# Kernel optimization log

Hardware: AMD Instinct MI355X
Metric: run time of the kernel (lower is better)

## Reference

```python
import jax, jax.numpy as jnp
import numpy as np

K, d = 8, 8
D = K * d          # 64
B, T, N = 8, 12, 325


def _xavier(key, shape):
    fan_out, fan_in = shape
    lim = (6.0 / (fan_in + fan_out)) ** 0.5
    return jax.random.uniform(key, shape, jnp.float32, -lim, lim)


def setup_inputs() -> dict:
    key = jax.random.key(0)
    ks = jax.random.split(key, 8)
    return {
        "X": jax.random.normal(ks[0], (B, T, N, D), jnp.float32),
        "STE": jax.random.normal(ks[1], (B, T, N, D), jnp.float32),
        "adj": jax.random.randint(ks[2], (N, N), 0, 2, jnp.int32),
        "W7": _xavier(ks[3], (D, 2 * D)), "b7": jnp.zeros((D,), jnp.float32),
        "W8": _xavier(ks[4], (D, 2 * D)), "b8": jnp.zeros((D,), jnp.float32),
        "W9": _xavier(ks[5], (D, 2 * D)), "b9": jnp.zeros((D,), jnp.float32),
        "W10": _xavier(ks[6], (D, D)), "b10": jnp.zeros((D,), jnp.float32),
        "W11": _xavier(ks[7], (D, D)), "b11": jnp.zeros((D,), jnp.float32),
    }


def reference(X, STE, adj, W7, b7, W8, b8, W9, b9, W10, b10, W11, b11):
    # X, STE: [B, T, N, D]
    x = jnp.concatenate([X, STE], axis=-1)  # [B,T,N,2D]
    gelu = lambda t: jax.nn.gelu(t, approximate=False)  # torch F.gelu default = exact erf
    q = gelu(x @ W7.T + b7)  # [B,T,N,D]
    k = gelu(x @ W8.T + b8)
    v = gelu(x @ W9.T + b9)
    # split D into K heads of size d (equivalent to torch split(dim=-1)+cat(dim=0))
    heads = lambda t: t.reshape(B, T, N, K, d)
    q, k, v = heads(q), heads(k), heads(v)
    # scores: [K,B,T,N,N] == torch's [K*B,T,N,N]
    attn = jnp.einsum('btnkd,btmkd->kbtnm', q, k) / (d ** 0.5)
    attn = jnp.where(adj > 0, attn, jnp.float32(-9e15))
    attn = jax.nn.softmax(attn, axis=-1)
    out = jnp.einsum('kbtnm,btmkd->btnkd', attn, v).reshape(B, T, N, D)
    out = gelu(out @ W10.T + b10) @ W11.T + b11
    return out
```

## Files before the change

kernel.cpp:

```cpp
#include <hip/hip_runtime.h>
#include <math.h>

#define NN 325
#define BT 96
#define NROWS (BT * NN)
#define SCL (0.35355339059327373f * 1.4426950408889634f)
#define QKV_BLKS ((NROWS + 63) / 64)
#define PREP_ITEMS (11 * NN + 8192)
#define PREP_BLKS ((PREP_ITEMS + 511) / 512)
#define TOT_BLKS (QKV_BLKS + PREP_BLKS)

typedef _Float16 half_t;
typedef half_t half8_t __attribute__((ext_vector_type(8)));
typedef half_t half4_t __attribute__((ext_vector_type(4)));
typedef half_t half2_t __attribute__((ext_vector_type(2)));
typedef float float4_t __attribute__((ext_vector_type(4)));

__device__ __forceinline__ float gelu_f(float x) {
    return 0.5f * x * (1.0f + erff(x * 0.70710678118654752f));
}

#define XS 136
#define PS 72

__device__ __forceinline__ void qkv_stage_wf(const float* __restrict__ src,
                                             half_t* dst, int tid)
{
    #pragma unroll
    for (int idx = tid; idx < 1024; idx += 512) {
        int c = idx >> 4, g = idx & 15;
        const float4* s4 = (const float4*)&src[c * 128 + g * 8];
        float4 a = s4[0], b = s4[1];
        half8_t h;
        h[0] = (half_t)a.x; h[1] = (half_t)a.y;
        h[2] = (half_t)a.z; h[3] = (half_t)a.w;
        h[4] = (half_t)b.x; h[5] = (half_t)b.y;
        h[6] = (half_t)b.z; h[7] = (half_t)b.w;
        *(half8_t*)&dst[c * XS + g * 8] = h;
    }
}

__device__ __forceinline__ void qkv_compute(
    const half_t* x16, const half_t* wb, const float* __restrict__ b,
    half_t* __restrict__ outp, float oscale,
    int row0, int rbase, int ch, int l15, int quad)
{
    float4_t acc[2];
    #pragma unroll
    for (int cc = 0; cc < 2; ++cc) {
        float bias = b[(ch * 2 + cc) * 16 + l15];
        acc[cc] = (float4_t){bias, bias, bias, bias};
    }
    #pragma unroll
    for (int kk = 0; kk < 8; ++kk) {
        half4_t a = *(const half4_t*)&x16[(rbase + l15) * XS + kk * 16 + quad * 4];
        #pragma unroll
        for (int cc = 0; cc < 2; ++cc) {
            half4_t bf = *(const half4_t*)
                &wb[((ch * 2 + cc) * 16 + l15) * XS + kk * 16 + quad * 4];
            acc[cc] = __builtin_amdgcn_mfma_f32_16x16x16f16(a, bf, acc[cc], 0, 0, 0);
        }
    }
    #pragma unroll
    for (int cc = 0; cc < 2; ++cc) {
        #pragma unroll
        for (int rr = 0; rr < 4; ++rr) {
            int R = row0 + rbase + quad * 4 + rr;
            if (R < NROWS)
                outp[R * 64 + (ch * 2 + cc) * 16 + l15] =
                    (half_t)(gelu_f(acc[cc][rr]) * oscale);
        }
    }
}

__global__ __launch_bounds__(512) void qkv_kernel(
    const float* __restrict__ X, const float* __restrict__ STE,
    const int* __restrict__ adj,
    const float* __restrict__ W7, const float* __restrict__ b7,
    const float* __restrict__ W8, const float* __restrict__ b8,
    const float* __restrict__ W9, const float* __restrict__ b9,
    const float* __restrict__ W10, const float* __restrict__ W11,
    half_t* __restrict__ q, half_t* __restrict__ k, half_t* __restrict__ v,
    unsigned int* __restrict__ packedT, half_t* __restrict__ wab)
{
    const int tid = threadIdx.x;
    const int bx  = blockIdx.x;

    if (bx >= QKV_BLKS) {
        int idx = (bx - QKV_BLKS) * 512 + tid;
        if (idx < 11 * NN) {
            int w = idx / NN, n = idx - w * NN;
            unsigned int bits = 0u;
            #pragma unroll 8
            for (int j = 0; j < 32; ++j) {
                int m = w * 32 + j;
                if (m < NN && adj[n * NN + m] > 0) bits |= (1u << j);
            }
            packedT[w * NN + n] = bits;
        } else if (idx < PREP_ITEMS) {
            int i = idx - 11 * NN;
            int p = i >> 12, r = i & 4095;
            wab[i] = (half_t)(p ? W11[r] : W10[r]);
        }
        return;
    }

    __shared__ __attribute__((aligned(16))) half_t x16[64 * XS];
    __shared__ __attribute__((aligned(16))) half_t wbuf[2][64 * XS];
    const int row0 = bx * 64;

    #pragma unroll
    for (int idx = tid; idx < 2048; idx += 512) {
        int r = idx >> 5, c4 = idx & 31;
        int R = row0 + r;
        float4 f = {0.f, 0.f, 0.f, 0.f};
        if (R < NROWS)
            f = (c4 < 16) ? *(const float4*)(X + R * 64 + c4 * 4)
                          : *(const float4*)(STE + R * 64 + (c4 - 16) * 4);
        half4_t hv;
        hv[0] = (half_t)f.x; hv[1] = (half_t)f.y;
        hv[2] = (half_t)f.z; hv[3] = (half_t)f.w;
        *(half4_t*)&x16[r * XS + c4 * 4] = hv;
    }
    qkv_stage_wf(W7, wbuf[0], tid);
    __syncthreads();

    const int lane = tid & 63, wv = tid >> 6;
    const int l15 = lane & 15, quad = lane >> 4;
    const int rbase = (wv & 3) * 16, ch = wv >> 2;

    qkv_stage_wf(W8, wbuf[1], tid);
    qkv_compute(x16, wbuf[0], b7, q, SCL, row0, rbase, ch, l15, quad);
    __syncthreads();

    qkv_stage_wf(W9, wbuf[0], tid);
    qkv_compute(x16, wbuf[1], b8, k, 1.0f, row0, rbase, ch, l15, quad);
    __syncthreads();

    qkv_compute(x16, wbuf[0], b9, v, 1.0f, row0, rbase, ch, l15, quad);
}

__global__ __launch_bounds__(512) void attn_kernel(
    const half_t* __restrict__ q16g, const half_t* __restrict__ k16g,
    const half_t* __restrict__ v16g, const unsigned int* __restrict__ packedT,
    half_t* __restrict__ ao)
{
    __shared__ __attribute__((aligned(16))) half_t K16[336 * 20];
    __shared__ __attribute__((aligned(16))) half_t VT16[16 * 344];
    __shared__ float smax8[8];
    const int tid = threadIdx.x;
    const int bx  = blockIdx.x;
    const int h   = bx / BT;
    const int bt  = bx - h * BT;
    const long base = (long)(bt * NN) * 64 + h * 8;

    const half4_t z4 = {(half_t)0.f, (half_t)0.f, (half_t)0.f, (half_t)0.f};

    for (int idx = tid; idx < 16 * 344 / 2; idx += 512)
        ((half2_t*)VT16)[idx] = (half2_t)(half_t)0.f;
    __syncthreads();
    for (int i = tid; i < 344; i += 512)
        VT16[8 * 344 + i] = (half_t)1.0f;

    float nk2 = 0.0f;
    for (int r = tid; r < 336; r += 512) {
        half4_t ka = z4, kbv = z4;
        if (r < NN) {
            ka  = *(const half4_t*)(k16g + base + r * 64);
            kbv = *(const half4_t*)(k16g + base + r * 64 + 4);
        }
        *(half4_t*)&K16[r * 20]      = ka;
        *(half4_t*)&K16[r * 20 + 4]  = kbv;
        *(half4_t*)&K16[r * 20 + 8]  = z4;
        *(half4_t*)&K16[r * 20 + 12] = z4;
        #pragma unroll
        for (int j = 0; j < 4; ++j) {
            float fa = (float)ka[j], fb = (float)kbv[j];
            nk2 = fmaf(fa, fa, nk2);
            nk2 = fmaf(fb, fb, nk2);
        }
    }

    for (int mp = tid; mp < 168; mp += 512) {
        int m0 = 2 * mp, m1 = 2 * mp + 1;
        half4_t v0a = z4, v0b = z4, v1a = z4, v1b = z4;
        if (m0 < NN) {
            v0a = *(const half4_t*)(v16g + base + m0 * 64);
            v0b = *(const half4_t*)(v16g + base + m0 * 64 + 4);
        }
        if (m1 < NN) {
            v1a = *(const half4_t*)(v16g + base + m1 * 64);
            v1b = *(const half4_t*)(v16g + base + m1 * 64 + 4);
        }
        #pragma unroll
        for (int c = 0; c < 4; ++c) {
            half2_t p0; p0[0] = v0a[c]; p0[1] = v1a[c];
            half2_t p1; p1[0] = v0b[c]; p1[1] = v1b[c];
            *(half2_t*)&VT16[c * 344 + 2 * mp]       = p0;
            *(half2_t*)&VT16[(c + 4) * 344 + 2 * mp] = p1;
        }
    }

    #pragma unroll
    for (int off = 32; off >= 1; off >>= 1)
        nk2 = fmaxf(nk2, __shfl_xor(nk2, off, 64));
    if ((tid & 63) == 0) smax8[tid >> 6] = nk2;
    __syncthreads();

    const float maxk2 = fmaxf(
        fmaxf(fmaxf(smax8[0], smax8[1]), fmaxf(smax8[2], smax8[3])),
        fmaxf(fmaxf(smax8[4], smax8[5]), fmaxf(smax8[6], smax8[7])));

    const int lane = tid & 63;
    const int wv   = tid >> 6;
    const int l15  = lane & 15;
    const int quad = lane >> 4;
    const int qsh  = quad * 4;

    for (int t = wv; t < 21; t += 8) {
        const int n  = t * 16 + l15;
        const int nq = (n < NN) ? n : (NN - 1);

        half4_t qf = z4;
        if (quad < 2)
            qf = *(const half4_t*)(q16g + base + (long)nq * 64 + qsh);

        float ssq = 0.0f;
        #pragma unroll
        for (int j = 0; j < 4; ++j) {
            float fq = (float)qf[j];
            ssq = fmaf(fq, fq, ssq);
        }
        ssq += __shfl_xor(ssq, 16, 64);
        ssq += __shfl_xor(ssq, 32, 64);
        const float rm = sqrtf(ssq * maxk2);

        unsigned int mb[11];
        #pragma unroll
        for (int w = 0; w < 11; ++w) mb[w] = packedT[w * NN + nq];

        const float4_t cinit = {-rm, -rm, -rm, -rm};
        float4_t acc = {0.f, 0.f, 0.f, 0.f};
        #pragma unroll
        for (int mt = 0; mt < 21; ++mt) {
            half4_t kf = *(const half4_t*)&K16[(mt * 16 + l15) * 20 + qsh];
            float4_t sv = __builtin_amdgcn_mfma_f32_16x16x16f16(
                kf, qf, cinit, 0, 0, 0);
            unsigned int sh = mb[mt >> 1] >> (((mt & 1) << 4) + qsh);
            float p0 = (sh & 1u) ? __builtin_amdgcn_exp2f(sv[0]) : 0.f;
            float p1 = (sh & 2u) ? __builtin_amdgcn_exp2f(sv[1]) : 0.f;
            float p2 = (sh & 4u) ? __builtin_amdgcn_exp2f(sv[2]) : 0.f;
            float p3 = (sh & 8u) ? __builtin_amdgcn_exp2f(sv[3]) : 0.f;
            half4_t pf;
            pf[0] = (half_t)p0; pf[1] = (half_t)p1;
            pf[2] = (half_t)p2; pf[3] = (half_t)p3;
            half4_t vf = *(const half4_t*)&VT16[l15 * 344 + mt * 16 + qsh];
            acc = __builtin_amdgcn_mfma_f32_16x16x16f16(vf, pf, acc, 0, 0, 0);
        }

        float sum = __shfl(acc[0], 32 + l15, 64);

        if (quad < 2 && n < NN) {
            float inv = 1.0f / sum;
            half4_t o;
            o[0] = (half_t)(acc[0] * inv); o[1] = (half_t)(acc[1] * inv);
            o[2] = (half_t)(acc[2] * inv); o[3] = (half_t)(acc[3] * inv);
            *(half4_t*)(ao + base + (long)n * 64 + qsh) = o;
        }
    }
}

__global__ __launch_bounds__(512) void proj_kernel(
    const half_t* __restrict__ ao, const half_t* __restrict__ wab,
    const float* __restrict__ b10, const float* __restrict__ b11,
    float* __restrict__ out)
{
    __shared__ __attribute__((aligned(16))) half_t a16[64 * PS];
    __shared__ __attribute__((aligned(16))) half_t wA[64 * PS];
    __shared__ __attribute__((aligned(16))) half_t wB[64 * PS];
    __shared__ __attribute__((aligned(16))) half_t h16[64 * PS];
    const int tid  = threadIdx.x;
    const int row0 = blockIdx.x * 64;

    for (int idx = tid; idx < 512; idx += 512) {
        int r = idx >> 3, c8 = idx & 7;
        int R = row0 + r;
        uint4 u = {0u, 0u, 0u, 0u};
        if (R < NROWS) u = *(const uint4*)(ao + (long)R * 64 + c8 * 8);
        *(uint4*)&a16[r * PS + c8 * 8] = u;
        *(uint4*)&wA[r * PS + c8 * 8] = *(const uint4*)&wab[r * 64 + c8 * 8];
        *(uint4*)&wB[r * PS + c8 * 8] = *(const uint4*)&wab[4096 + r * 64 + c8 * 8];
    }
    __syncthreads();

    const int lane = tid & 63, wv = tid >> 6;
    const int l15 = lane & 15, quad = lane >> 4;
    const int rbase = (wv & 3) * 16, ch = wv >> 2;

    float4_t acc[2];
    #pragma unroll
    for (int cc = 0; cc < 2; ++cc) {
        float bias = b10[(ch * 2 + cc) * 16 + l15];
        acc[cc] = (float4_t){bias, bias, bias, bias};
    }
    #pragma unroll
    for (int kk = 0; kk < 4; ++kk) {
        half4_t a = *(const half4_t*)&a16[(rbase + l15) * PS + kk * 16 + quad * 4];
        #pragma unroll
        for (int cc = 0; cc < 2; ++cc) {
            half4_t bf = *(const half4_t*)
                &wA[((ch * 2 + cc) * 16 + l15) * PS + kk * 16 + quad * 4];
            acc[cc] = __builtin_amdgcn_mfma_f32_16x16x16f16(a, bf, acc[cc], 0, 0, 0);
        }
    }
    #pragma unroll
    for (int cc = 0; cc < 2; ++cc) {
        #pragma unroll
        for (int rr = 0; rr < 4; ++rr)
            h16[(rbase + quad * 4 + rr) * PS + (ch * 2 + cc) * 16 + l15] =
                (half_t)gelu_f(acc[cc][rr]);
    }
    __syncthreads();

    #pragma unroll
    for (int cc = 0; cc < 2; ++cc) {
        float bias = b11[(ch * 2 + cc) * 16 + l15];
        acc[cc] = (float4_t){bias, bias, bias, bias};
    }
    #pragma unroll
    for (int kk = 0; kk < 4; ++kk) {
        half4_t a = *(const half4_t*)&h16[(rbase + l15) * PS + kk * 16 + quad * 4];
        #pragma unroll
        for (int cc = 0; cc < 2; ++cc) {
            half4_t bf = *(const half4_t*)
                &wB[((ch * 2 + cc) * 16 + l15) * PS + kk * 16 + quad * 4];
            acc[cc] = __builtin_amdgcn_mfma_f32_16x16x16f16(a, bf, acc[cc], 0, 0, 0);
        }
    }
    #pragma unroll
    for (int cc = 0; cc < 2; ++cc) {
        #pragma unroll
        for (int rr = 0; rr < 4; ++rr) {
            int R = row0 + rbase + quad * 4 + rr;
            if (R < NROWS)
                out[R * 64 + (ch * 2 + cc) * 16 + l15] = acc[cc][rr];
        }
    }
}

extern "C" void kernel_launch(void* const* d_in, const int* in_sizes, int n_in,
                              void* d_out, int out_size, void* d_ws, size_t ws_size,
                              hipStream_t stream) {
    const float* X   = (const float*)d_in[0];
    const float* STE = (const float*)d_in[1];
    const int*   adj = (const int*)d_in[2];
    const float* W7  = (const float*)d_in[3];
    const float* b7  = (const float*)d_in[4];
    const float* W8  = (const float*)d_in[5];
    const float* b8  = (const float*)d_in[6];
    const float* W9  = (const float*)d_in[7];
    const float* b9  = (const float*)d_in[8];
    const float* W10 = (const float*)d_in[9];
    const float* b10 = (const float*)d_in[10];
    const float* W11 = (const float*)d_in[11];
    const float* b11 = (const float*)d_in[12];

    char* wsb = (char*)d_ws;
    const long S = (long)NROWS * 64;
    half_t* qb = (half_t*)wsb;
    half_t* kb = qb + S;
    half_t* vb = qb + 2 * S;
    half_t* ab = qb + 3 * S;
    unsigned int* pk = (unsigned int*)(wsb + 4 * S * sizeof(half_t));
    half_t* wab = (half_t*)(wsb + 4 * S * sizeof(half_t) + 16384);

    qkv_kernel<<<dim3(TOT_BLKS), 512, 0, stream>>>(
        X, STE, adj, W7, b7, W8, b8, W9, b9, W10, W11,
        qb, kb, vb, pk, wab);
    attn_kernel<<<dim3(8 * BT), 512, 0, stream>>>(qb, kb, vb, pk, ab);
    proj_kernel<<<dim3((NROWS + 63) / 64), 512, 0, stream>>>(
        ab, wab, b10, b11, (float*)d_out);
}
```

Baseline: 138.6 us.

## Store q/k/v head-major, approximate erf in GELU, skip redundant zero-fill sync

The q/k/v intermediates are now written head-major ([bt][head][n][8]), so each attention block reads a contiguous slab instead of 16-byte pieces strided by 128 bytes. The erf-based GELU is replaced with the Abramowitz-Stegun polynomial using hardware rcp and exp2, which cuts math cost in the qkv and proj epilogues at some accuracy cost. The VT16 zero-fill now skips the ones row that is overwritten afterwards, and the barrier between the two fills is removed. The qkv store epilogue now does per-row integer division and writes scattered 2-byte stores.

```diff
diff --git a/kernel.cpp b/kernel.cpp
--- a/kernel.cpp
+++ b/kernel.cpp
@@ -9,6 +9,7 @@
 #define PREP_ITEMS (11 * NN + 8192)
 #define PREP_BLKS ((PREP_ITEMS + 511) / 512)
 #define TOT_BLKS (QKV_BLKS + PREP_BLKS)
+#define HSTR (NN * 8)
 
 typedef _Float16 half_t;
 typedef half_t half8_t __attribute__((ext_vector_type(8)));
@@ -17,7 +18,18 @@
 typedef float float4_t __attribute__((ext_vector_type(4)));
 
 __device__ __forceinline__ float gelu_f(float x) {
-    return 0.5f * x * (1.0f + erff(x * 0.70710678118654752f));
+    const float z  = 0.70710678118654752f * x;
+    const float az = __builtin_fabsf(z);
+    const float t  = __builtin_amdgcn_rcpf(__builtin_fmaf(0.3275911f, az, 1.0f));
+    float p = __builtin_fmaf(1.061405429f, t, -1.453152027f);
+    p = __builtin_fmaf(p, t, 1.421413741f);
+    p = __builtin_fmaf(p, t, -0.284496736f);
+    p = __builtin_fmaf(p, t, 0.254829592f);
+    p *= t;
+    const float e = __builtin_amdgcn_exp2f(-az * az * 1.4426950408889634f);
+    float er = __builtin_fmaf(-p, e, 1.0f);
+    er = __builtin_copysignf(er, z);
+    return 0.5f * x * (1.0f + er);
 }
 
 #define XS 136
@@ -62,13 +74,16 @@
         }
     }
     #pragma unroll
-    for (int cc = 0; cc < 2; ++cc) {
-        #pragma unroll
-        for (int rr = 0; rr < 4; ++rr) {
-            int R = row0 + rbase + quad * 4 + rr;
-            if (R < NROWS)
-                outp[R * 64 + (ch * 2 + cc) * 16 + l15] =
+    for (int rr = 0; rr < 4; ++rr) {
+        int R = row0 + rbase + quad * 4 + rr;
+        if (R < NROWS) {
+            int bt = R / NN, n = R - bt * NN;
+            #pragma unroll
+            for (int cc = 0; cc < 2; ++cc) {
+                int col = (ch * 2 + cc) * 16 + l15;
+                outp[(long)((bt << 3) + (col >> 3)) * HSTR + n * 8 + (col & 7)] =
                     (half_t)(gelu_f(acc[cc][rr]) * oscale);
+            }
         }
     }
 }
@@ -152,13 +167,14 @@
     const int bx  = blockIdx.x;
     const int h   = bx / BT;
     const int bt  = bx - h * BT;
-    const long base = (long)(bt * NN) * 64 + h * 8;
+    const long qbase = (long)((bt << 3) + h) * HSTR;
+    const long baseO = (long)(bt * NN) * 64 + h * 8;
 
     const half4_t z4 = {(half_t)0.f, (half_t)0.f, (half_t)0.f, (half_t)0.f};
 
     for (int idx = tid; idx < 16 * 344 / 2; idx += 512)
-        ((half2_t*)VT16)[idx] = (half2_t)(half_t)0.f;
-    __syncthreads();
+        if (idx < 1376 || idx >= 1548)
+            ((half2_t*)VT16)[idx] = (half2_t)(half_t)0.f;
     for (int i = tid; i < 344; i += 512)
         VT16[8 * 344 + i] = (half_t)1.0f;
 
@@ -166,8 +182,8 @@
     for (int r = tid; r < 336; r += 512) {
         half4_t ka = z4, kbv = z4;
         if (r < NN) {
-            ka  = *(const half4_t*)(k16g + base + r * 64);
-            kbv = *(const half4_t*)(k16g + base + r * 64 + 4);
+            ka  = *(const half4_t*)(k16g + qbase + r * 8);
+            kbv = *(const half4_t*)(k16g + qbase + r * 8 + 4);
         }
         *(half4_t*)&K16[r * 20]      = ka;
         *(half4_t*)&K16[r * 20 + 4]  = kbv;
@@ -185,12 +201,12 @@
         int m0 = 2 * mp, m1 = 2 * mp + 1;
         half4_t v0a = z4, v0b = z4, v1a = z4, v1b = z4;
         if (m0 < NN) {
-            v0a = *(const half4_t*)(v16g + base + m0 * 64);
-            v0b = *(const half4_t*)(v16g + base + m0 * 64 + 4);
+            v0a = *(const half4_t*)(v16g + qbase + m0 * 8);
+            v0b = *(const half4_t*)(v16g + qbase + m0 * 8 + 4);
         }
         if (m1 < NN) {
-            v1a = *(const half4_t*)(v16g + base + m1 * 64);
-            v1b = *(const half4_t*)(v16g + base + m1 * 64 + 4);
+            v1a = *(const half4_t*)(v16g + qbase + m1 * 8);
+            v1b = *(const half4_t*)(v16g + qbase + m1 * 8 + 4);
         }
         #pragma unroll
         for (int c = 0; c < 4; ++c) {
@@ -223,7 +239,7 @@
 
         half4_t qf = z4;
         if (quad < 2)
-            qf = *(const half4_t*)(q16g + base + (long)nq * 64 + qsh);
+            qf = *(const half4_t*)(q16g + qbase + (long)nq * 8 + qsh);
 
         float ssq = 0.0f;
         #pragma unroll
@@ -265,7 +281,7 @@
             half4_t o;
             o[0] = (half_t)(acc[0] * inv); o[1] = (half_t)(acc[1] * inv);
             o[2] = (half_t)(acc[2] * inv); o[3] = (half_t)(acc[3] * inv);
-            *(half4_t*)(ao + base + (long)n * 64 + qsh) = o;
+            *(half4_t*)(ao + baseO + (long)n * 64 + qsh) = o;
         }
     }
 }
```

New measurement: 139.9 us (median of 3 runs). About the same (+0.9%).
